# Kernel optimization log

Measured on AMD Instinct MI355X. Metric: run time of the kernel, lower is better.

## Reference

```python
import jax, jax.numpy as jnp
from jax import lax
import numpy as np

POINT_PAIRS = 10000
SIGMA = 0.03
ALPHA = 1.0
MIN_DEPTH = -0.001
MAX_DEPTH = 80.0


def _get_edges(images):
    # images: [n,3,H,W]; Sobel on channel 0, VALID conv then zero-pad by 1 (as in torch code)
    x = images[:, :1]
    kx = jnp.array([[-1., 0., 1.], [-2., 0., 2.], [-1., 0., 1.]], jnp.float32).reshape(1, 1, 3, 3)
    ky = jnp.array([[1., 2., 1.], [0., 0., 0.], [-1., -2., -1.]], jnp.float32).reshape(1, 1, 3, 3)
    gx = lax.conv_general_dilated(x, kx, (1, 1), 'VALID')
    gy = lax.conv_general_dilated(x, ky, (1, 1), 'VALID')
    edges = jnp.sqrt(gx * gx + gy * gy)
    thetas = jnp.arctan2(gy, gx)
    pad = ((0, 0), (0, 0), (1, 1), (1, 1))
    return jnp.pad(edges, pad), jnp.pad(thetas, pad)


def _sample_and_loss(key, inp, tgt, edge, theta, smask):
    # inp/tgt/edge/theta: [H,W] float; smask: [H,W] bool
    H, W = inp.shape
    k1, k2, k3 = jax.random.split(key, 3)
    # edge-guided anchor sampling: uniform over {edge >= 0.1*max} & strict_mask, with replacement
    emask = (edge >= 0.1 * edge.max()) & smask
    p = emask.reshape(-1).astype(jnp.float32)
    p = p / jnp.maximum(p.sum(), 1.0)
    flat_idx = jax.random.choice(k1, H * W, (POINT_PAIRS,), replace=True, p=p)
    sh = flat_idx // W
    sw = flat_idx % W
    th = theta.reshape(-1)[flat_idx]
    # signed step distances along / perpendicular to the edge direction
    dist = jax.random.randint(k2, (4, POINT_PAIRS), 2, 31).astype(jnp.float32)
    sign = jnp.array([-1., -1., 1., 1.], jnp.float32).reshape(4, 1)
    dist = dist * sign
    # random_direct: p<0.5 -> along gradient; else rotate theta by pi/2 (swapped cos/sin)
    pdir = jax.random.uniform(k3) < 0.5
    th2 = ((th + jnp.pi / 2) + jnp.pi) % (2 * jnp.pi) - jnp.pi
    col1 = sw[None, :] + jnp.round(dist * jnp.cos(th)[None, :]).astype(jnp.int32)
    row1 = sh[None, :] + jnp.round(dist * jnp.sin(th)[None, :]).astype(jnp.int32)
    col2 = sw[None, :] + jnp.round(dist * jnp.sin(th2)[None, :]).astype(jnp.int32)
    row2 = sh[None, :] + jnp.round(dist * jnp.cos(th2)[None, :]).astype(jnp.int32)
    col = jnp.where(pdir, col1, col2)  # [4,N]
    row = jnp.where(pdir, row1, row2)
    inb = (col >= 0) & (col <= W - 1) & (row >= 0) & (row <= H - 1)
    valid = jnp.all(inb, axis=0)  # [N]; torch drops these columns, we mask instead
    colc = jnp.clip(col, 0, W - 1)
    rowc = jnp.clip(row, 0, H - 1)
    # pairs (a,b),(b,c),(c,d) -> A = [a,b,c], B = [b,c,d]
    rA = jnp.concatenate([rowc[0], rowc[1], rowc[2]])
    cA = jnp.concatenate([colc[0], colc[1], colc[2]])
    rB = jnp.concatenate([rowc[1], rowc[2], rowc[3]])
    cB = jnp.concatenate([colc[1], colc[2], colc[3]])
    vm = jnp.concatenate([valid, valid, valid]).astype(jnp.float32)  # [3N]
    iA = inp[rA, cA]
    iB = inp[rB, cB]
    tA = tgt[rA, cA]
    tB = tgt[rB, cB]
    # ranking loss
    ratio = (tA + 1e-6) / (tB + 1e-6)
    absdiff = jnp.abs(tA - tB)
    maxdiff = jnp.max(jnp.where(vm > 0, absdiff, 0.0))
    tw = jnp.exp(absdiff / (maxdiff + 1e-6))
    eq = (ratio < 1.0 + SIGMA) & (ratio > 1.0 / (1.0 + SIGMA))
    labels = jnp.where(ratio >= 1.0 + SIGMA, 1.0,
                       jnp.where(ratio <= 1.0 / (1.0 + SIGMA), -1.0, 0.0))
    equal_loss = (iA - iB) ** 2 / tw * eq.astype(jnp.float32)
    unequal_loss = jnp.log1p(jnp.exp((iB - iA) * labels)) * (1.0 - eq.astype(jnp.float32))
    cnt = jnp.maximum(vm.sum(), 1.0)
    loss = ALPHA * jnp.sum(equal_loss * vm) / cnt + jnp.sum(unequal_loss * vm) / cnt
    return loss, vm.sum()


def setup_inputs() -> dict:
    key = jax.random.key(0)
    k1, k2, k3, k4 = jax.random.split(key, 4)
    n, H, W = 8, 1024, 1024
    inputs = jax.random.normal(k1, (n, 1, H, W), jnp.float32)
    targets = jax.random.uniform(k2, (n, 1, H, W), jnp.float32)
    images = jax.random.uniform(k3, (n, 3, H, W), jnp.float32)
    depth_gt = jax.random.uniform(k4, (n, 1, H, W), jnp.float32)
    return {"inputs": inputs, "targets": targets, "images": images, "depth_gt": depth_gt}


def reference(inputs, targets, images, depth_gt):
    n = inputs.shape[0]
    strict = (depth_gt > MIN_DEPTH) & (depth_gt < MAX_DEPTH) & ~(targets == 80.0)
    edges, thetas = _get_edges(images)
    keys = jax.random.split(jax.random.key(42), n)
    losses, counts = jax.vmap(_sample_and_loss)(
        keys, inputs[:, 0], targets[:, 0], edges[:, 0], thetas[:, 0], strict[:, 0])
    return losses.sum() / n, counts.sum() / n
```

## Files before the change

### kernel.cpp

```cpp
#include <hip/hip_runtime.h>
#include <math.h>
#include <stdint.h>

#define NIMG 8
#define HH 1024
#define WW 1024
#define NPIX (HH*WW)
#define PAIRS 10000
#define STRIP 8
#define NSTRIPS 128
#define S1BLOCKS 40
#define SEGCAP 30000

#define OFF_EDGE 0
#define OFF_MDI  4096
#define OFF_DONE 4352
#define OFF_UN   4608
#define OFF_CNT  4864
#define OFF_SEGC 5120
#define OFF_GL   5376
#define OFF_GC   5408
#define OFF_IMGD 5440
#define ZERO_N   1376

__device__ __forceinline__ uint64_t mix64(uint64_t x){
    x += 0x9E3779B97F4A7C15ull;
    x = (x ^ (x >> 30)) * 0xBF58476D1CE4E5B9ull;
    x = (x ^ (x >> 27)) * 0x94D049BB133111EBull;
    return x ^ (x >> 31);
}

__device__ __forceinline__ float block_reduce_max(float v, float* sm){
    for (int off = 32; off; off >>= 1)
        v = fmaxf(v, __shfl_down(v, off));
    int wv = threadIdx.x >> 6, lane = threadIdx.x & 63;
    if (lane == 0) sm[wv] = v;
    __syncthreads();
    if (threadIdx.x == 0)
        sm[0] = fmaxf(fmaxf(sm[0], sm[1]), fmaxf(sm[2], sm[3]));
    __syncthreads();
    float r = sm[0];
    __syncthreads();
    return r;
}

__device__ __forceinline__ float block_reduce_sum(float v, float* sm){
    for (int off = 32; off; off >>= 1)
        v += __shfl_down(v, off);
    int wv = threadIdx.x >> 6, lane = threadIdx.x & 63;
    if (lane == 0) sm[wv] = v;
    __syncthreads();
    if (threadIdx.x == 0)
        sm[0] = sm[0] + sm[1] + sm[2] + sm[3];
    __syncthreads();
    float r = sm[0];
    __syncthreads();
    return r;
}

__device__ __forceinline__ void load16(const float* __restrict__ p, float* d){
    const float4* q = (const float4*)p;
    float4 v0 = q[0], v1 = q[1], v2 = q[2], v3 = q[3];
    d[0]=v0.x; d[1]=v0.y; d[2]=v0.z; d[3]=v0.w;
    d[4]=v1.x; d[5]=v1.y; d[6]=v1.z; d[7]=v1.w;
    d[8]=v2.x; d[9]=v2.y; d[10]=v2.z; d[11]=v2.w;
    d[12]=v3.x; d[13]=v3.y; d[14]=v3.z; d[15]=v3.w;
}

__global__ __launch_bounds__(256) void edgemax_kernel(const float* __restrict__ images,
                                                      float* __restrict__ ws){
    if (blockIdx.x == 0){
        for (int i = threadIdx.x; i < ZERO_N; i += 256)
            ws[OFF_MDI + i] = 0.0f;
    }

    int img  = blockIdx.x & 7;
    int xb   = blockIdx.x >> 3;
    const float* x = images + (size_t)img * 3 * NPIX;
    int wv   = threadIdx.x >> 6;
    int lane = threadIdx.x & 63;
    int strip = xb * 4 + wv;
    int r0 = 1 + strip * STRIP;
    int r1 = min(r0 + STRIP - 1, HH - 2);
    int c0 = lane * 16;

    float a[16], b[16], n[16];
    load16(x + (size_t)(r0-1)*WW + c0, a);
    load16(x + (size_t)r0*WW + c0, b);

    float m = 0.0f;
    for (int r = r0; r <= r1; ++r){
        load16(x + (size_t)(r+1)*WW + c0, n);
        float sx[16], dy[16];
        #pragma unroll
        for (int i = 0; i < 16; ++i){
            sx[i] = a[i] + 2.0f*b[i] + n[i];
            dy[i] = a[i] - n[i];
        }
        float sxl = __shfl_up(sx[15], 1);
        float sxr = __shfl_down(sx[0], 1);
        float dyl = __shfl_up(dy[15], 1);
        float dyr = __shfl_down(dy[0], 1);
        #pragma unroll
        for (int j = 0; j < 16; ++j){
            float sl = (j == 0)  ? sxl : sx[j-1];
            float sr = (j == 15) ? sxr : sx[j+1];
            float dl = (j == 0)  ? dyl : dy[j-1];
            float dr = (j == 15) ? dyr : dy[j+1];
            float gx = sr - sl;
            float gy = dl + 2.0f*dy[j] + dr;
            float e2 = gx*gx + gy*gy;
            int c = c0 + j;
            if (c >= 1 && c <= WW-2) m = fmaxf(m, e2);
        }
        #pragma unroll
        for (int i = 0; i < 16; ++i){ a[i] = b[i]; b[i] = n[i]; }
    }
    for (int off = 32; off; off >>= 1)
        m = fmaxf(m, __shfl_down(m, off));
    if (lane == 0)
        ws[OFF_EDGE + img * NSTRIPS + strip] = m;
}

struct AttLd {
    int r, c, rl, cl;
    float a, b, cc, d, e, f, g, h, dg, tg;
};

__device__ __forceinline__ AttLd att_issue(uint64_t u,
        const float* __restrict__ x, const float* __restrict__ tgt,
        const float* __restrict__ dgt){
    AttLd s;
    uint32_t pix = (uint32_t)(u >> 44);
    s.r  = (int)(pix >> 10);
    s.c  = (int)(pix & (WW - 1));
    s.rl = min(max(s.r, 1), HH-2);
    s.cl = min(max(s.c, 1), WW-2);
    const float* p0 = x + (size_t)(s.rl-1)*WW + s.cl;
    const float* p1 = x + (size_t)s.rl*WW + s.cl;
    const float* p2 = x + (size_t)(s.rl+1)*WW + s.cl;
    s.a = p0[-1]; s.b = p0[0]; s.cc = p0[1];
    s.d = p1[-1];               s.e = p1[1];
    s.f = p2[-1]; s.g = p2[0];  s.h = p2[1];
    s.dg = dgt[s.rl*WW + s.cl];
    s.tg = tgt[s.rl*WW + s.cl];
    return s;
}

__global__ __launch_bounds__(256) void sample_finish_kernel(
                               const float* __restrict__ inputs,
                               const float* __restrict__ targets,
                               const float* __restrict__ images,
                               const float* __restrict__ depth_gt,
                               float* __restrict__ ws,
                               unsigned long long* __restrict__ segs,
                               float* __restrict__ out){
    __shared__ float sred[4];
    __shared__ unsigned flag1;
    int img  = blockIdx.x & 7;
    int jb   = blockIdx.x >> 3;
    int tid  = threadIdx.x;
    int lane = tid & 63;
    int j    = jb * 256 + tid;
    const float* x   = images   + (size_t)img * 3 * NPIX;
    const float* inp = inputs   + (size_t)img * NPIX;
    const float* tgt = targets  + (size_t)img * NPIX;
    const float* dgt = depth_gt + (size_t)img * NPIX;

    float ev = 0.0f;
    if (tid < NSTRIPS) ev = ws[OFF_EDGE + img * NSTRIPS + tid];
    float thr2 = 0.01f * block_reduce_max(ev, sred);

    float mdiff = 0.0f, un = 0.0f, cntv = 0.0f;
    float d2a[3] = {0.f,0.f,0.f}, ada[3] = {0.f,0.f,0.f};
    bool  eqf[3] = {false,false,false};

    if (j < PAIRS){
        uint64_t base = ((uint64_t)(img * PAIRS + j)) << 10;
        bool pdir = (mix64(((uint64_t)(NIMG * PAIRS + img)) << 10) & 1ull) != 0ull;

        int sh = -1, sw = -1;
        float gxs = 0.f, gys = 0.f, e2s = 1.f;

        AttLd cur = att_issue(mix64(base + 0ull), x, tgt, dgt);
        for (int att = 0; att < 900; ++att){
            AttLd nxt = att_issue(mix64(base + (uint64_t)(att + 1)), x, tgt, dgt);
            float gx = (cur.cc - cur.a) + 2.0f*(cur.e - cur.d) + (cur.h - cur.f);
            float gy = (cur.a + 2.0f*cur.b + cur.cc) - (cur.f + 2.0f*cur.g + cur.h);
            float e2 = gx*gx + gy*gy;
            bool pass = (cur.r == cur.rl) && (cur.c == cur.cl) && (e2 >= thr2) &&
                        (cur.dg > -0.001f && cur.dg < 80.0f) && (cur.tg != 80.0f);
            if (pass){
                sh = cur.rl; sw = cur.cl; gxs = gx; gys = gy; e2s = e2;
                break;
            }
            cur = nxt;
        }

        if (sh >= 0){
            float inv = rsqrtf(e2s);
            float cmul = gxs * inv;
            float rmul = gys * inv;
            if (!pdir) cmul = -cmul;

            uint64_t u0 = mix64(base + 1000ull);
            uint64_t u1 = mix64(base + 1001ull);
            float dist[4];
            dist[0] = -(float)(2u + (uint32_t)(u0 & 0xFFFFFFFFull) % 29u);
            dist[1] = -(float)(2u + (uint32_t)(u0 >> 32) % 29u);
            dist[2] =  (float)(2u + (uint32_t)(u1 & 0xFFFFFFFFull) % 29u);
            dist[3] =  (float)(2u + (uint32_t)(u1 >> 32) % 29u);

            int rowc[4], colc[4];
            bool valid = true;
            #pragma unroll
            for (int k = 0; k < 4; ++k){
                int cc2 = sw + (int)rintf(dist[k] * cmul);
                int rr2 = sh + (int)rintf(dist[k] * rmul);
                if (cc2 < 0 || cc2 > WW-1 || rr2 < 0 || rr2 > HH-1) valid = false;
                colc[k] = min(max(cc2, 0), WW-1);
                rowc[k] = min(max(rr2, 0), HH-1);
            }

            if (valid){
                float t4[4], i4[4];
                #pragma unroll
                for (int k = 0; k < 4; ++k){
                    int p = rowc[k]*WW + colc[k];
                    t4[k] = tgt[p];
                    i4[k] = inp[p];
                }
                #pragma unroll
                for (int k = 0; k < 3; ++k){
                    float tA = t4[k], tB = t4[k+1];
                    float ratio = (tA + 1e-6f) / (tB + 1e-6f);
                    float adk = fabsf(tA - tB);
                    mdiff = fmaxf(mdiff, adk);
                    bool eq = (ratio < 1.03f) && (ratio > 0.9708737864077669f);
                    if (eq){
                        float d = i4[k] - i4[k+1];
                        d2a[k] = d*d; ada[k] = adk; eqf[k] = true;
                    } else {
                        float lab = (ratio >= 1.03f) ? 1.0f : -1.0f;
                        un += log1pf(expf((i4[k+1] - i4[k]) * lab));
                    }
                }
                cntv = 3.0f;
            }
        }
    }

    {
        unsigned long long m0 = __ballot(eqf[0]);
        unsigned long long m1 = __ballot(eqf[1]);
        unsigned long long m2 = __ballot(eqf[2]);
        int c0 = __popcll(m0), c1 = __popcll(m1), c2 = __popcll(m2);
        int wavetot = c0 + c1 + c2;
        unsigned basei = 0;
        if (lane == 0 && wavetot)
            basei = atomicAdd((unsigned int*)&ws[OFF_SEGC + img*32],
                              (unsigned)wavetot);
        basei = (unsigned)__shfl((int)basei, 0);
        unsigned long long below = (1ull << lane) - 1ull;
        unsigned long long* sp = segs + (size_t)img * SEGCAP;
        #pragma unroll
        for (int k = 0; k < 3; ++k){
            if (eqf[k]){
                unsigned off = basei
                    + (k > 0 ? (unsigned)c0 : 0u)
                    + (k > 1 ? (unsigned)c1 : 0u)
                    + (unsigned)__popcll(((k==0)?m0:(k==1)?m1:m2) & below);
                unsigned long long v = ((unsigned long long)__float_as_uint(ada[k]) << 32)
                                     | (unsigned long long)__float_as_uint(d2a[k]);
                atomicExch(&sp[off], v);
            }
        }
    }

    float mdb = block_reduce_max(mdiff, sred);
    float unb = block_reduce_sum(un, sred);
    float cnb = block_reduce_sum(cntv, sred);
    if (tid == 0){
        if (mdb > 0.0f)
            atomicMax((unsigned int*)&ws[OFF_MDI + img*32], __float_as_uint(mdb));
        atomicAdd(&ws[OFF_UN  + img*32], unb);
        atomicAdd(&ws[OFF_CNT + img*32], cnb);
        asm volatile("s_waitcnt vmcnt(0)" ::: "memory");
        unsigned old = atomicAdd((unsigned int*)&ws[OFF_DONE + img*32], 1u);
        flag1 = (old == (unsigned)(S1BLOCKS - 1)) ? 1u : 0u;
    }
    __syncthreads();

    if (flag1){
        float md = __uint_as_float(
            atomicAdd((unsigned int*)&ws[OFF_MDI + img*32], 0u));
        float inv = 1.0f / (md + 1e-6f);
        unsigned nseg = atomicAdd((unsigned int*)&ws[OFF_SEGC + img*32], 0u);
        unsigned long long* sp = segs + (size_t)img * SEGCAP;

        float eqs = 0.0f;
        for (unsigned r = tid; r < nseg; r += 256){
            unsigned long long v = atomicAdd(&sp[r], 0ull);
            float d2v = __uint_as_float((unsigned)(v & 0xFFFFFFFFull));
            float adv = __uint_as_float((unsigned)(v >> 32));
            eqs += d2v * expf(-adv * inv);
        }
        eqs = block_reduce_sum(eqs, sred);

        if (tid == 0){
            float unv = atomicAdd(&ws[OFF_UN  + img*32], 0.0f);
            float cnv = atomicAdd(&ws[OFF_CNT + img*32], 0.0f);
            float Li = (eqs + unv) / fmaxf(cnv, 1.0f);
            atomicAdd(&ws[OFF_GL], Li);
            atomicAdd(&ws[OFF_GC], cnv);
            asm volatile("s_waitcnt vmcnt(0)" ::: "memory");
            unsigned o2 = atomicAdd((unsigned int*)&ws[OFF_IMGD], 1u);
            if (o2 == (unsigned)(NIMG - 1)){
                float gl = atomicAdd(&ws[OFF_GL], 0.0f);
                float gc = atomicAdd(&ws[OFF_GC], 0.0f);
                out[0] = gl / (float)NIMG;
                out[1] = gc / (float)NIMG;
            }
        }
    }
}

extern "C" void kernel_launch(void* const* d_in, const int* in_sizes, int n_in,
                              void* d_out, int out_size, void* d_ws, size_t ws_size,
                              hipStream_t stream) {
    const float* inputs  = (const float*)d_in[0];
    const float* targets = (const float*)d_in[1];
    const float* images  = (const float*)d_in[2];
    const float* depth   = (const float*)d_in[3];
    float* out = (float*)d_out;

    float* ws = (float*)d_ws;
    unsigned long long* segs = (unsigned long long*)((char*)d_ws + 65536);

    hipLaunchKernelGGL(edgemax_kernel, dim3(NSTRIPS/4 * NIMG), dim3(256), 0, stream,
                       images, ws);
    hipLaunchKernelGGL(sample_finish_kernel, dim3(S1BLOCKS * NIMG), dim3(256), 0, stream,
                       inputs, targets, images, depth, ws, segs, out);
}
```

Before: 36.90 us.

## Use single-wave blocks for sampling kernel and finer edge-max strips

```diff
diff --git a/kernel.cpp b/kernel.cpp
--- a/kernel.cpp
+++ b/kernel.cpp
@@ -7,9 +7,9 @@
 #define WW 1024
 #define NPIX (HH*WW)
 #define PAIRS 10000
-#define STRIP 8
-#define NSTRIPS 128
-#define S1BLOCKS 40
+#define STRIP 4
+#define NSTRIPS 256
+#define SBLK 157
 #define SEGCAP 30000
 
 #define OFF_EDGE 0
@@ -30,32 +30,16 @@
     return x ^ (x >> 31);
 }
 
-__device__ __forceinline__ float block_reduce_max(float v, float* sm){
+__device__ __forceinline__ float wave_reduce_max(float v){
     for (int off = 32; off; off >>= 1)
         v = fmaxf(v, __shfl_down(v, off));
-    int wv = threadIdx.x >> 6, lane = threadIdx.x & 63;
-    if (lane == 0) sm[wv] = v;
-    __syncthreads();
-    if (threadIdx.x == 0)
-        sm[0] = fmaxf(fmaxf(sm[0], sm[1]), fmaxf(sm[2], sm[3]));
-    __syncthreads();
-    float r = sm[0];
-    __syncthreads();
-    return r;
-}
-
-__device__ __forceinline__ float block_reduce_sum(float v, float* sm){
+    return __shfl(v, 0);
+}
+
+__device__ __forceinline__ float wave_reduce_sum(float v){
     for (int off = 32; off; off >>= 1)
         v += __shfl_down(v, off);
-    int wv = threadIdx.x >> 6, lane = threadIdx.x & 63;
-    if (lane == 0) sm[wv] = v;
-    __syncthreads();
-    if (threadIdx.x == 0)
-        sm[0] = sm[0] + sm[1] + sm[2] + sm[3];
-    __syncthreads();
-    float r = sm[0];
-    __syncthreads();
-    return r;
+    return __shfl(v, 0);
 }
 
 __device__ __forceinline__ void load16(const float* __restrict__ p, float* d){
@@ -147,7 +131,7 @@
     return s;
 }
 
-__global__ __launch_bounds__(256) void sample_finish_kernel(
+__global__ __launch_bounds__(64) void sample_finish_kernel(
                                const float* __restrict__ inputs,
                                const float* __restrict__ targets,
                                const float* __restrict__ images,
@@ -155,21 +139,20 @@
                                float* __restrict__ ws,
                                unsigned long long* __restrict__ segs,
                                float* __restrict__ out){
-    __shared__ float sred[4];
-    __shared__ unsigned flag1;
     int img  = blockIdx.x & 7;
     int jb   = blockIdx.x >> 3;
-    int tid  = threadIdx.x;
-    int lane = tid & 63;
-    int j    = jb * 256 + tid;
+    int lane = threadIdx.x;
+    int j    = jb * 64 + lane;
     const float* x   = images   + (size_t)img * 3 * NPIX;
     const float* inp = inputs   + (size_t)img * NPIX;
     const float* tgt = targets  + (size_t)img * NPIX;
     const float* dgt = depth_gt + (size_t)img * NPIX;
 
     float ev = 0.0f;
-    if (tid < NSTRIPS) ev = ws[OFF_EDGE + img * NSTRIPS + tid];
-    float thr2 = 0.01f * block_reduce_max(ev, sred);
+    #pragma unroll
+    for (int s = 0; s < 4; ++s)
+        ev = fmaxf(ev, ws[OFF_EDGE + img * NSTRIPS + lane + s*64]);
+    float thr2 = 0.01f * wave_reduce_max(ev);
 
     float mdiff = 0.0f, un = 0.0f, cntv = 0.0f;
     float d2a[3] = {0.f,0.f,0.f}, ada[3] = {0.f,0.f,0.f};
@@ -277,21 +260,22 @@
         }
     }
 
-    float mdb = block_reduce_max(mdiff, sred);
-    float unb = block_reduce_sum(un, sred);
-    float cnb = block_reduce_sum(cntv, sred);
-    if (tid == 0){
+    float mdb = wave_reduce_max(mdiff);
+    float unb = wave_reduce_sum(un);
+    float cnb = wave_reduce_sum(cntv);
+    int isLast = 0;
+    if (lane == 0){
         if (mdb > 0.0f)
             atomicMax((unsigned int*)&ws[OFF_MDI + img*32], __float_as_uint(mdb));
         atomicAdd(&ws[OFF_UN  + img*32], unb);
         atomicAdd(&ws[OFF_CNT + img*32], cnb);
         asm volatile("s_waitcnt vmcnt(0)" ::: "memory");
         unsigned old = atomicAdd((unsigned int*)&ws[OFF_DONE + img*32], 1u);
-        flag1 = (old == (unsigned)(S1BLOCKS - 1)) ? 1u : 0u;
-    }
-    __syncthreads();
-
-    if (flag1){
+        isLast = (old == (unsigned)(SBLK - 1)) ? 1 : 0;
+    }
+    isLast = __shfl(isLast, 0);
+
+    if (isLast){
         float md = __uint_as_float(
             atomicAdd((unsigned int*)&ws[OFF_MDI + img*32], 0u));
         float inv = 1.0f / (md + 1e-6f);
@@ -299,15 +283,15 @@
         unsigned long long* sp = segs + (size_t)img * SEGCAP;
 
         float eqs = 0.0f;
-        for (unsigned r = tid; r < nseg; r += 256){
+        for (unsigned r = lane; r < nseg; r += 64){
             unsigned long long v = atomicAdd(&sp[r], 0ull);
             float d2v = __uint_as_float((unsigned)(v & 0xFFFFFFFFull));
             float adv = __uint_as_float((unsigned)(v >> 32));
             eqs += d2v * expf(-adv * inv);
         }
-        eqs = block_reduce_sum(eqs, sred);
-
-        if (tid == 0){
+        eqs = wave_reduce_sum(eqs);
+
+        if (lane == 0){
             float unv = atomicAdd(&ws[OFF_UN  + img*32], 0.0f);
             float cnv = atomicAdd(&ws[OFF_CNT + img*32], 0.0f);
             float Li = (eqs + unv) / fmaxf(cnv, 1.0f);
@@ -339,6 +323,6 @@
 
     hipLaunchKernelGGL(edgemax_kernel, dim3(NSTRIPS/4 * NIMG), dim3(256), 0, stream,
                        images, ws);
-    hipLaunchKernelGGL(sample_finish_kernel, dim3(S1BLOCKS * NIMG), dim3(256), 0, stream,
+    hipLaunchKernelGGL(sample_finish_kernel, dim3(SBLK * NIMG), dim3(64), 0, stream,
                        inputs, targets, images, depth, ws, segs, out);
 }
```

Result: slower. 39.50 us (+7.0%).
